# Kernel optimization log

Measured on AMD Instinct MI355X. Metric: run time of the kernel, lower is better.

## Reference

```python
import jax, jax.numpy as jnp
import numpy as np

N = 8192        # nodes
E = 262144      # edges (avg degree 32)
IN_CH = 256
CH = 128
SLOPE = 0.2     # PyG GATv2Conv default negative_slope


def gatv2(x, src, dst, wl, wr, att, b):
    """Single-head GATv2Conv (PyG defaults: share_weights=False, self-loops
    already appended to src/dst). x: [N, in]; wl, wr: [out, in]; att: [out]."""
    xl = x @ wl.T                      # [N, out] source-side transform (x_j)
    xr = x @ wr.T                      # [N, out] target-side transform (x_i)
    # per-edge attention logit: att . LeakyReLU(x_l[src] + x_r[dst])
    e = jax.nn.leaky_relu(xl[src] + xr[dst], SLOPE) @ att   # [E']
    # segment softmax over incoming edges of each target node
    m = jax.ops.segment_max(e, dst, num_segments=N)
    p = jnp.exp(e - m[dst])
    s = jax.ops.segment_sum(p, dst, num_segments=N)
    alpha = p / s[dst]                 # every node has a self-loop -> s > 0
    out = jax.ops.segment_sum(alpha[:, None] * xl[src], dst, num_segments=N)
    return out + b


def setup_inputs() -> dict:
    key = jax.random.key(0)
    ks = jax.random.split(key, 2 + 5 * 3)
    inp = {
        "x": jax.random.normal(ks[0], (N, IN_CH), dtype=jnp.float32),
        "edge_index": jax.random.randint(ks[1], (2, E), 0, N, dtype=jnp.int64),
    }
    dims = [(CH, IN_CH), (2 * CH, CH), (CH, 2 * CH), (CH, 2 * CH), (IN_CH, CH)]
    ki = 2
    for i, (oc, ic) in enumerate(dims, start=1):
        sc = (2.0 / (ic + oc)) ** 0.5  # glorot-ish
        inp[f"w{i}l"] = jax.random.normal(ks[ki], (oc, ic), dtype=jnp.float32) * sc
        inp[f"w{i}r"] = jax.random.normal(ks[ki + 1], (oc, ic), dtype=jnp.float32) * sc
        inp[f"a{i}"] = jax.random.normal(ks[ki + 2], (oc,), dtype=jnp.float32) * sc
        inp[f"b{i}"] = jnp.zeros((oc,), dtype=jnp.float32)
        ki += 3
    return inp


def reference(x, edge_index,
              w1l, w1r, a1, b1,
              w2l, w2r, a2, b2,
              w3l, w3r, a3, b3,
              w4l, w4r, a4, b4,
              w5l, w5r, a5, b5):
    loops = jnp.arange(N, dtype=edge_index.dtype)
    src = jnp.concatenate([edge_index[0], loops])   # add_self_loops=True
    dst = jnp.concatenate([edge_index[1], loops])
    h = jax.nn.relu(gatv2(x, src, dst, w1l, w1r, a1, b1))          # [N, CH]
    z = jax.nn.relu(gatv2(h, src, dst, w2l, w2r, a2, b2))          # [N, 2CH]
    re = jax.nn.relu(gatv2(z, src, dst, w3l, w3r, a3, b3))         # [N, CH]
    recon_edge = jax.nn.sigmoid(re @ re.T)                         # [N, N]
    xd = jax.nn.relu(gatv2(z, src, dst, w4l, w4r, a4, b4))         # [N, CH]
    x_rec = jax.nn.relu(gatv2(xd, src, dst, w5l, w5r, a5, b5))     # [N, IN_CH]
    return recon_edge, x_rec, z
```

## Files before the change

kernel.cpp:

```cpp
#include <hip/hip_runtime.h>
#include <hip/hip_bf16.h>
#include <math.h>

#define N_NODES 8192
#define N_EDGES 262144
#define EP (N_EDGES + N_NODES)
#define SLOPE 0.2f

typedef short bf16x8 __attribute__((ext_vector_type(8)));
typedef short short4v __attribute__((ext_vector_type(4)));
typedef float f32x4 __attribute__((ext_vector_type(4)));

__global__ void extract_hist(const int* __restrict__ raw,
                             int* __restrict__ esrc, int* __restrict__ edst,
                             int* __restrict__ counts) {
    __shared__ int sflag;
    int t = threadIdx.x;
    if (t < 64) {
        unsigned long long b = __ballot(raw[2 * t + 1] != 0);
        if (t == 0) sflag = (b == 0ULL) ? 1 : 0;
    }
    __syncthreads();
    int i64f = sflag;
    int k = blockIdx.x * blockDim.x + t;
    if (k >= N_EDGES) return;
    int s, d;
    if (i64f) {
        s = raw[2 * (size_t)k];
        d = raw[2 * ((size_t)N_EDGES + k)];
    } else {
        s = raw[k];
        d = raw[N_EDGES + k];
    }
    esrc[k] = s;
    edst[k] = d;
    atomicAdd(&counts[d], 1);
}

__global__ void scan_k(const int* __restrict__ counts, int* __restrict__ row_ptr) {
    __shared__ int part[256];
    int t = threadIdx.x;
    int base = t * 32;
    int loc[32];
    int s = 0;
    for (int i = 0; i < 32; ++i) { loc[i] = s; s += counts[base + i] + 1; }
    part[t] = s;
    __syncthreads();
    for (int off = 1; off < 256; off <<= 1) {
        int tmp = (t >= off) ? part[t - off] : 0;
        __syncthreads();
        part[t] += tmp;
        __syncthreads();
    }
    int incl = part[t];
    int excl = incl - s;
    for (int i = 0; i < 32; ++i) row_ptr[base + i] = excl + loc[i];
    if (t == 255) row_ptr[N_NODES] = incl;
}

__global__ void scatter_k(const int* __restrict__ esrc, const int* __restrict__ edst,
                          const int* __restrict__ row_ptr, int* __restrict__ cursor,
                          int* __restrict__ ssrc) {
    int k = blockIdx.x * blockDim.x + threadIdx.x;
    if (k >= EP) return;
    int s, d;
    if (k < N_EDGES) { s = esrc[k]; d = edst[k]; }
    else             { s = d = k - N_EDGES; }
    int pos = row_ptr[d] + atomicAdd(&cursor[d], 1);
    ssrc[pos] = s;
}

struct WPrep {
    const float* wl[5];
    const float* wr[5];
    int oc[5];
    int lk[5];
};

__global__ void prep_all(WPrep P, const float* __restrict__ x,
                         short* __restrict__ W3all, short* __restrict__ A3) {
    int gid = blockIdx.x * blockDim.x + threadIdx.x;
    if (gid < 524288) {
        int r = gid >> 6;
        int c4 = (gid & 63) << 2;
        f32x4 a = *(const f32x4*)&x[((size_t)r << 8) + c4];
        short4v h4, l4;
#pragma unroll
        for (int j = 0; j < 4; ++j) {
            __hip_bfloat16 hb = __float2bfloat16(a[j]);
            float hf = __bfloat162float(hb);
            __hip_bfloat16 lb = __float2bfloat16(a[j] - hf);
            h4[j] = *(short*)&hb;
            l4[j] = *(short*)&lb;
        }
        size_t ro = (size_t)r * 768;
        *(short4v*)&A3[ro + c4] = h4;
        *(short4v*)&A3[ro + 256 + c4] = l4;
        *(short4v*)&A3[ro + 512 + c4] = h4;
    } else {
        int g = gid - 524288;
        int l = g >> 16;
        if (l >= 5) return;
        int rem = g & 65535;
        int lk = P.lk[l], K = 1 << lk;
        int r = rem >> lk, c = rem & (K - 1);
        int OC = P.oc[l];
        const float* w = (r < OC) ? P.wl[l] : P.wr[l];
        int rr = (r < OC) ? r : r - OC;
        float a = w[((size_t)rr << lk) + c];
        __hip_bfloat16 hb = __float2bfloat16(a);
        float hf = __bfloat162float(hb);
        __hip_bfloat16 lb = __float2bfloat16(a - hf);
        size_t ro = (size_t)l * 196608 + (size_t)r * 3 * K;
        W3all[ro + c] = *(short*)&hb;
        W3all[ro + K + c] = *(short*)&hb;
        W3all[ro + 2 * K + c] = *(short*)&lb;
    }
}

#if __has_builtin(__builtin_amdgcn_global_load_lds)
#define GL16(gsrc, lbase, lofs)                                                       \
    __builtin_amdgcn_global_load_lds((const __attribute__((address_space(1))) void*)(gsrc), \
                                     (__attribute__((address_space(3))) void*)(lbase), 16, 0, 0)
#else
#define GL16(gsrc, lbase, lofs) (*(bf16x8*)((lbase) + (lofs)) = *(const bf16x8*)(gsrc))
#endif

__global__ __launch_bounds__(256) void gemm_bf16_nt(const short* __restrict__ A3,
                                                    const short* __restrict__ W3,
                                                    float* __restrict__ XL,
                                                    float* __restrict__ XR,
                                                    int K3, int N2, int OC) {
    __shared__ __align__(16) short As[2][4096];
    __shared__ __align__(16) short Bs[2][4096];
    int tid = threadIdx.x;
    int gx = gridDim.x;
    int lgx = (gx == 8) ? 3 : 2;
    int orig = blockIdx.x + (blockIdx.y << lgx);
    int nwg = gx << 7;
    int swzb = (orig & 7) * (nwg >> 3) + (orig >> 3);
    int bx = swzb & (gx - 1), by = swzb >> lgx;
    int i0 = by * 64, j0 = bx * 64;

    int wave = tid >> 6, lane = tid & 63;
    int b0 = wave * 1024 + lane * 16;
    int row0 = b0 >> 7;
    int rb0 = b0 & 127;
    int scb = rb0 ^ ((row0 & 7) << 4);
    const short* gA0 = A3 + (size_t)(i0 + row0) * K3 + (scb >> 1);
    const short* gA1 = A3 + (size_t)(i0 + row0 + 32) * K3 + (scb >> 1);
    const short* gB0 = W3 + (size_t)(j0 + row0) * K3 + (scb >> 1);
    const short* gB1 = W3 + (size_t)(j0 + row0 + 32) * K3 + (scb >> 1);
    int lofs = lane * 8;

#define STAGE(pb, k0s)                                      \
    do {                                                    \
        GL16(gA0 + (k0s), &As[pb][wave * 512], lofs);       \
        GL16(gA1 + (k0s), &As[pb][2048 + wave * 512], lofs);\
        GL16(gB0 + (k0s), &Bs[pb][wave * 512], lofs);       \
        GL16(gB1 + (k0s), &Bs[pb][2048 + wave * 512], lofs);\
    } while (0)

    int wr = (wave >> 1) * 32, wc = (wave & 1) * 32;
    int lm = lane & 15, quad = lane >> 4;
    f32x4 acc[2][2] = {};
    int nt = K3 >> 6;
    STAGE(0, 0);
    int cur = 0;
    for (int t = 0; t < nt; ++t) {
        if (t + 1 < nt) {
            STAGE(cur ^ 1, (t + 1) << 6);
            asm volatile("s_waitcnt vmcnt(4)" ::: "memory");
        } else {
            asm volatile("s_waitcnt vmcnt(0)" ::: "memory");
        }
        __builtin_amdgcn_s_barrier();
        __builtin_amdgcn_sched_barrier(0);
        const char* Ab = (const char*)&As[cur][0];
        const char* Bb = (const char*)&Bs[cur][0];
#pragma unroll
        for (int ks = 0; ks < 2; ++ks) {
            int kb = ks * 64 + quad * 16;
            bf16x8 a[2], b[2];
#pragma unroll
            for (int u = 0; u < 2; ++u) {
                int r = wr + u * 16 + lm;
                a[u] = *(const bf16x8*)(Ab + (((r << 7) | kb) ^ ((r & 7) << 4)));
            }
#pragma unroll
            for (int v = 0; v < 2; ++v) {
                int r = wc + v * 16 + lm;
                b[v] = *(const bf16x8*)(Bb + (((r << 7) | kb) ^ ((r & 7) << 4)));
            }
#pragma unroll
            for (int u = 0; u < 2; ++u)
#pragma unroll
                for (int v = 0; v < 2; ++v)
                    acc[u][v] = __builtin_amdgcn_mfma_f32_16x16x32_bf16(a[u], b[v], acc[u][v], 0, 0, 0);
        }
        __builtin_amdgcn_sched_barrier(0);
        __builtin_amdgcn_s_barrier();
        cur ^= 1;
    }
#undef STAGE
    float* Cb;
    int col0;
    if (j0 < OC) { Cb = XL; col0 = j0; } else { Cb = XR; col0 = j0 - OC; }
#pragma unroll
    for (int u = 0; u < 2; ++u)
#pragma unroll
        for (int v = 0; v < 2; ++v)
#pragma unroll
            for (int r = 0; r < 4; ++r) {
                int row = i0 + wr + u * 16 + quad * 4 + r;
                int col = col0 + wc + v * 16 + lm;
                Cb[(size_t)row * OC + col] = acc[u][v][r];
            }
}

#define LSTR 136

__global__ __launch_bounds__(256) void recon_sym(const unsigned short* __restrict__ Rb,
                                                 float* __restrict__ C) {
    __shared__ __align__(16) short Sh[2 * 128 * LSTR];
    short* As = Sh;
    short* Bs = Sh + 128 * LSTR;
    int tid = threadIdx.x;
    int orig = blockIdx.x;
    int s = (orig & 7) * 260 + (orig >> 3);
    float ff = 64.5f - sqrtf(64.5f * 64.5f - 2.0f * (float)s);
    int bi = (int)ff;
    while (bi > 0 && 64 * bi - bi * (bi - 1) / 2 > s) --bi;
    while (64 * (bi + 1) - (bi + 1) * bi / 2 <= s) ++bi;
    int bj = bi + (s - (64 * bi - bi * (bi - 1) / 2));
    int i0 = bi * 128, j0 = bj * 128;
    const short* R = (const short*)Rb;
#pragma unroll
    for (int c = 0; c < 8; ++c) {
        int idx = tid + c * 256;
        int row = idx >> 4, col = (idx & 15) * 8;
        *(bf16x8*)(&As[row * LSTR + col]) = *(const bf16x8*)(&R[(size_t)(i0 + row) * 128 + col]);
        *(bf16x8*)(&Bs[row * LSTR + col]) = *(const bf16x8*)(&R[(size_t)(j0 + row) * 128 + col]);
    }
    __syncthreads();
    int wave = tid >> 6, lane = tid & 63;
    int wr = (wave >> 1) * 64, wc = (wave & 1) * 64;
    int lm = lane & 15, quad = lane >> 4;
    f32x4 acc[4][4] = {};
#pragma unroll
    for (int ks = 0; ks < 4; ++ks) {
        int ko = ks * 32 + quad * 8;
        bf16x8 a[4], b[4];
#pragma unroll
        for (int u = 0; u < 4; ++u)
            a[u] = *(const bf16x8*)(&As[(wr + u * 16 + lm) * LSTR + ko]);
#pragma unroll
        for (int v = 0; v < 4; ++v)
            b[v] = *(const bf16x8*)(&Bs[(wc + v * 16 + lm) * LSTR + ko]);
#pragma unroll
        for (int u = 0; u < 4; ++u)
#pragma unroll
            for (int v = 0; v < 4; ++v)
                acc[u][v] = __builtin_amdgcn_mfma_f32_16x16x32_bf16(a[u], b[v], acc[u][v], 0, 0, 0);
    }
#pragma unroll
    for (int u = 0; u < 4; ++u)
#pragma unroll
        for (int v = 0; v < 4; ++v)
#pragma unroll
            for (int r = 0; r < 4; ++r) {
                acc[u][v][r] = 1.0f / (1.0f + __expf(-acc[u][v][r]));
                int row = i0 + wr + u * 16 + quad * 4 + r;
                int col = j0 + wc + v * 16 + lm;
                C[(size_t)row * 8192 + col] = acc[u][v][r];
            }
    if (bi != bj) {
        __syncthreads();
        float* T = (float*)Sh;
#pragma unroll
        for (int u = 0; u < 4; ++u)
#pragma unroll
            for (int v = 0; v < 4; ++v)
#pragma unroll
                for (int r = 0; r < 4; ++r)
                    T[(wr + u * 16 + quad * 4 + r) * 129 + (wc + v * 16 + lm)] = acc[u][v][r];
        __syncthreads();
#pragma unroll
        for (int it = 0; it < 64; ++it) {
            int idx = tid + it * 256;
            int rp = idx >> 7, cp = idx & 127;
            C[(size_t)(j0 + rp) * 8192 + (i0 + cp)] = T[cp * 129 + rp];
        }
    }
}

__global__ __launch_bounds__(256) void gat_node256(const int* __restrict__ row_ptr,
                                                   const int* __restrict__ ssrc,
                                                   const float* __restrict__ XL,
                                                   const float* __restrict__ XR,
                                                   const float* __restrict__ att,
                                                   const float* __restrict__ bias,
                                                   float* __restrict__ outf,
                                                   short* __restrict__ a3) {
    __shared__ float sacc[4][256];
    __shared__ float sm[4], ss[4];
    int d = blockIdx.x, t = threadIdx.x;
    int lane = t & 63, wave = t >> 6;
    int beg = row_ptr[d], end = row_ptr[d + 1];
    f32x4 xr = *(const f32x4*)&XR[(size_t)d * 256 + lane * 4];
    f32x4 at = *(const f32x4*)&att[lane * 4];
    float m = -INFINITY, s = 0.0f;
    f32x4 acc = {0.0f, 0.0f, 0.0f, 0.0f};
    int p = beg + wave;
    for (; p + 4 < end; p += 8) {
        int s0 = ssrc[p], s1 = ssrc[p + 4];
        f32x4 v0 = *(const f32x4*)&XL[(size_t)s0 * 256 + lane * 4];
        f32x4 v1 = *(const f32x4*)&XL[(size_t)s1 * 256 + lane * 4];
        float e0 = 0.0f, e1 = 0.0f;
#pragma unroll
        for (int j = 0; j < 4; ++j) {
            float u0 = v0[j] + xr[j]; u0 = (u0 > 0.0f) ? u0 : SLOPE * u0; e0 += u0 * at[j];
            float u1 = v1[j] + xr[j]; u1 = (u1 > 0.0f) ? u1 : SLOPE * u1; e1 += u1 * at[j];
        }
#pragma unroll
        for (int off = 32; off; off >>= 1) {
            e0 += __shfl_xor(e0, off, 64);
            e1 += __shfl_xor(e1, off, 64);
        }
        float mn = fmaxf(m, fmaxf(e0, e1));
        float f = __expf(m - mn), q0 = __expf(e0 - mn), q1 = __expf(e1 - mn);
        s = s * f + q0 + q1;
#pragma unroll
        for (int j = 0; j < 4; ++j) acc[j] = acc[j] * f + q0 * v0[j] + q1 * v1[j];
        m = mn;
    }
    if (p < end) {
        int si = ssrc[p];
        f32x4 v = *(const f32x4*)&XL[(size_t)si * 256 + lane * 4];
        float e = 0.0f;
#pragma unroll
        for (int j = 0; j < 4; ++j) {
            float u = v[j] + xr[j];
            u = (u > 0.0f) ? u : SLOPE * u;
            e += u * at[j];
        }
#pragma unroll
        for (int off = 32; off; off >>= 1) e += __shfl_xor(e, off, 64);
        float mn = fmaxf(m, e);
        float f = __expf(m - mn), p0 = __expf(e - mn);
        s = s * f + p0;
#pragma unroll
        for (int j = 0; j < 4; ++j) acc[j] = acc[j] * f + p0 * v[j];
        m = mn;
    }
    *(f32x4*)&sacc[wave][lane * 4] = acc;
    if (lane == 0) { sm[wave] = m; ss[wave] = s; }
    __syncthreads();
    float M = fmaxf(fmaxf(sm[0], sm[1]), fmaxf(sm[2], sm[3]));
    float tot = 0.0f, st = 0.0f;
#pragma unroll
    for (int w = 0; w < 4; ++w) {
        float fw = __expf(sm[w] - M);
        tot += sacc[w][t] * fw;
        st += ss[w] * fw;
    }
    float val = fmaxf(tot / st + bias[t], 0.0f);
    if (outf) outf[(size_t)d * 256 + t] = val;
    if (a3) {
        __hip_bfloat16 hb = __float2bfloat16(val);
        float hf = __bfloat162float(hb);
        __hip_bfloat16 lb = __float2bfloat16(val - hf);
        size_t ro = (size_t)d * 768;
        a3[ro + t] = *(short*)&hb;
        a3[ro + 256 + t] = *(short*)&lb;
        a3[ro + 512 + t] = *(short*)&hb;
    }
}

__global__ __launch_bounds__(256) void gat_node128(const int* __restrict__ row_ptr,
                                                   const int* __restrict__ ssrc,
                                                   const float* __restrict__ XL,
                                                   const float* __restrict__ XR,
                                                   const float* __restrict__ att,
                                                   const float* __restrict__ bias,
                                                   float* __restrict__ outf,
                                                   short* __restrict__ a3,
                                                   unsigned short* __restrict__ rb) {
    __shared__ float sacc[8][128];
    __shared__ float sm[8], ss[8];
    int d = blockIdx.x, t = threadIdx.x;
    int ln = t & 31, hw = t >> 5;
    int beg = row_ptr[d], end = row_ptr[d + 1];
    f32x4 xr = *(const f32x4*)&XR[(size_t)d * 128 + ln * 4];
    f32x4 at = *(const f32x4*)&att[ln * 4];
    float m = -INFINITY, s = 0.0f;
    f32x4 acc = {0.0f, 0.0f, 0.0f, 0.0f};
    int p = beg + hw;
    for (; p + 8 < end; p += 16) {
        int s0 = ssrc[p], s1 = ssrc[p + 8];
        f32x4 v0 = *(const f32x4*)&XL[(size_t)s0 * 128 + ln * 4];
        f32x4 v1 = *(const f32x4*)&XL[(size_t)s1 * 128 + ln * 4];
        float e0 = 0.0f, e1 = 0.0f;
#pragma unroll
        for (int j = 0; j < 4; ++j) {
            float u0 = v0[j] + xr[j]; u0 = (u0 > 0.0f) ? u0 : SLOPE * u0; e0 += u0 * at[j];
            float u1 = v1[j] + xr[j]; u1 = (u1 > 0.0f) ? u1 : SLOPE * u1; e1 += u1 * at[j];
        }
#pragma unroll
        for (int off = 16; off; off >>= 1) {
            e0 += __shfl_xor(e0, off, 32);
            e1 += __shfl_xor(e1, off, 32);
        }
        float mn = fmaxf(m, fmaxf(e0, e1));
        float f = __expf(m - mn), q0 = __expf(e0 - mn), q1 = __expf(e1 - mn);
        s = s * f + q0 + q1;
#pragma unroll
        for (int j = 0; j < 4; ++j) acc[j] = acc[j] * f + q0 * v0[j] + q1 * v1[j];
        m = mn;
    }
    if (p < end) {
        int si = ssrc[p];
        f32x4 v = *(const f32x4*)&XL[(size_t)si * 128 + ln * 4];
        float e = 0.0f;
#pragma unroll
        for (int j = 0; j < 4; ++j) {
            float u = v[j] + xr[j];
            u = (u > 0.0f) ? u : SLOPE * u;
            e += u * at[j];
        }
#pragma unroll
        for (int off = 16; off; off >>= 1) e += __shfl_xor(e, off, 32);
        float mn = fmaxf(m, e);
        float f = __expf(m - mn), p0 = __expf(e - mn);
        s = s * f + p0;
#pragma unroll
        for (int j = 0; j < 4; ++j) acc[j] = acc[j] * f + p0 * v[j];
        m = mn;
    }
    *(f32x4*)&sacc[hw][ln * 4] = acc;
    if (ln == 0) { sm[hw] = m; ss[hw] = s; }
    __syncthreads();
    if (t < 128) {
        float M = sm[0];
#pragma unroll
        for (int w = 1; w < 8; ++w) M = fmaxf(M, sm[w]);
        float tot = 0.0f, st = 0.0f;
#pragma unroll
        for (int w = 0; w < 8; ++w) {
            float fw = __expf(sm[w] - M);
            tot += sacc[w][t] * fw;
            st += ss[w] * fw;
        }
        float val = fmaxf(tot / st + bias[t], 0.0f);
        if (outf) outf[(size_t)d * 128 + t] = val;
        if (a3) {
            __hip_bfloat16 hb = __float2bfloat16(val);
            float hf = __bfloat162float(hb);
            __hip_bfloat16 lb = __float2bfloat16(val - hf);
            size_t ro = (size_t)d * 384;
            a3[ro + t] = *(short*)&hb;
            a3[ro + 128 + t] = *(short*)&lb;
            a3[ro + 256 + t] = *(short*)&hb;
        }
        if (rb) {
            __hip_bfloat16 hb = __float2bfloat16(val);
            rb[d * 128 + t] = *(unsigned short*)&hb;
        }
    }
}

static inline int ceil_div(int a, int b) { return (a + b - 1) / b; }

extern "C" void kernel_launch(void* const* d_in, const int* in_sizes, int n_in,
                              void* d_out, int out_size, void* d_ws, size_t ws_size,
                              hipStream_t stream) {
    const float* x    = (const float*)d_in[0];
    const int*   eraw = (const int*)d_in[1];

    WPrep P;
    const float* att[5];
    const float* bia[5];
    for (int l = 0; l < 5; ++l) {
        P.wl[l] = (const float*)d_in[2 + 4 * l + 0];
        P.wr[l] = (const float*)d_in[2 + 4 * l + 1];
        att[l]  = (const float*)d_in[2 + 4 * l + 2];
        bia[l]  = (const float*)d_in[2 + 4 * l + 3];
    }
    const int och[5]  = {128, 256, 128, 128, 256};
    const int logK[5] = {8, 7, 8, 8, 7};
    for (int l = 0; l < 5; ++l) { P.oc[l] = och[l]; P.lk[l] = logK[l]; }

    float* outp  = (float*)d_out;
    float* recon = outp;
    float* xrec  = outp + (size_t)67108864;
    float* zout  = outp + (size_t)69206016;

    float* W = (float*)d_ws;
    float* XL    = W;
    float* XR    = W + 2097152;
    short* A3    = (short*)(W + 4194304);
    short* W3all = (short*)(W + 7340032);
    unsigned short* Rb = (unsigned short*)(W + 7831552);
    int* I       = (int*)(W + 8355840);
    int* counts  = I;
    int* cursor  = I + 8192;
    int* row_ptr = I + 16384;
    int* ssrc    = I + 24577;
    int* esrc    = I + 294913;
    int* edst    = I + 557057;

    hipMemsetAsync(counts, 0, 2 * 8192 * sizeof(int), stream);
    extract_hist<<<ceil_div(N_EDGES, 256), 256, 0, stream>>>(eraw, esrc, edst, counts);
    scan_k<<<1, 256, 0, stream>>>(counts, row_ptr);
    scatter_k<<<ceil_div(EP, 256), 256, 0, stream>>>(esrc, edst, row_ptr, cursor, ssrc);

    prep_all<<<3328, 256, 0, stream>>>(P, x, W3all, A3);

    for (int l = 0; l < 5; ++l) {
        int lk = logK[l], OC = och[l];
        int N2 = OC << 1, K3 = 3 << lk;

        dim3 g(N2 / 64, N_NODES / 64);
        gemm_bf16_nt<<<g, 256, 0, stream>>>(A3, W3all + (size_t)l * 196608, XL, XR, K3, N2, OC);

        if (OC == 128) {
            float* of = nullptr;
            short* a3 = (l == 0 || l == 3) ? A3 : nullptr;
            unsigned short* rb = (l == 2) ? Rb : nullptr;
            gat_node128<<<N_NODES, 256, 0, stream>>>(row_ptr, ssrc, XL, XR, att[l], bia[l], of, a3, rb);
        } else {
            float* of = (l == 1) ? zout : xrec;
            short* a3 = (l == 1) ? A3 : nullptr;
            gat_node256<<<N_NODES, 256, 0, stream>>>(row_ptr, ssrc, XL, XR, att[l], bia[l], of, a3);
        }

        if (l == 2) {
            recon_sym<<<2080, 256, 0, stream>>>(Rb, recon);
        }
    }
}
```

Baseline: 557.9 us.

## Merge layer-3/4 GEMMs, batch their GAT passes, drop softmax max tracking

Layers 3 and 4 both read z, so their projections now run as one wider GEMM whose weights sit next to each other in memory. Their two 128-channel attention passes run in a single launch that picks per-layer parameters from the block index. The GEMM now writes XL and XR side by side in one strided buffer, so the GAT kernels read both through offsets. The online-softmax running max and its rescaling are removed, and the code exponentiates the raw logits. That saves exp and FMA work per edge but risks overflow or precision loss if the logits get large.

Measured after the change: 534.8 us. 4.1% less time.

```diff
diff --git a/kernel.cpp b/kernel.cpp
--- a/kernel.cpp
+++ b/kernel.cpp
@@ -128,9 +128,8 @@
 
 __global__ __launch_bounds__(256) void gemm_bf16_nt(const short* __restrict__ A3,
                                                     const short* __restrict__ W3,
-                                                    float* __restrict__ XL,
-                                                    float* __restrict__ XR,
-                                                    int K3, int N2, int OC) {
+                                                    float* __restrict__ C,
+                                                    int K3, int N2) {
     __shared__ __align__(16) short As[2][4096];
     __shared__ __align__(16) short Bs[2][4096];
     int tid = threadIdx.x;
@@ -203,9 +202,6 @@
         cur ^= 1;
     }
 #undef STAGE
-    float* Cb;
-    int col0;
-    if (j0 < OC) { Cb = XL; col0 = j0; } else { Cb = XR; col0 = j0 - OC; }
 #pragma unroll
     for (int u = 0; u < 2; ++u)
 #pragma unroll
@@ -213,8 +209,8 @@
 #pragma unroll
             for (int r = 0; r < 4; ++r) {
                 int row = i0 + wr + u * 16 + quad * 4 + r;
-                int col = col0 + wc + v * 16 + lm;
-                Cb[(size_t)row * OC + col] = acc[u][v][r];
+                int col = j0 + wc + v * 16 + lm;
+                C[(size_t)row * N2 + col] = acc[u][v][r];
             }
 }
 
@@ -294,28 +290,113 @@
     }
 }
 
-__global__ __launch_bounds__(256) void gat_node256(const int* __restrict__ row_ptr,
-                                                   const int* __restrict__ ssrc,
-                                                   const float* __restrict__ XL,
-                                                   const float* __restrict__ XR,
-                                                   const float* __restrict__ att,
-                                                   const float* __restrict__ bias,
-                                                   float* __restrict__ outf,
-                                                   short* __restrict__ a3) {
+struct GatP {
+    const float* att; const float* bias;
+    float* outf; short* a3; unsigned short* rb;
+    int xlo, xro;
+};
+
+__global__ __launch_bounds__(256) void gat128(const int* __restrict__ row_ptr,
+                                              const int* __restrict__ ssrc,
+                                              const float* __restrict__ XLR, int str,
+                                              GatP P0, GatP P1) {
+    __shared__ float sacc[8][128];
+    __shared__ float ss[8];
+    int d = blockIdx.x & (N_NODES - 1);
+    GatP P = (blockIdx.x >= N_NODES) ? P1 : P0;
+    int t = threadIdx.x, ln = t & 31, hw = t >> 5;
+    int beg = row_ptr[d], end = row_ptr[d + 1];
+    const float* XL = XLR + P.xlo;
+    f32x4 at = *(const f32x4*)&P.att[ln * 4];
+    f32x4 xr = *(const f32x4*)&XLR[(size_t)d * str + P.xro + ln * 4];
+    float s = 0.0f;
+    f32x4 acc = {0.0f, 0.0f, 0.0f, 0.0f};
+    int p = beg + hw;
+    for (; p + 8 < end; p += 16) {
+        int s0 = ssrc[p], s1 = ssrc[p + 8];
+        f32x4 v0 = *(const f32x4*)&XL[(size_t)s0 * str + ln * 4];
+        f32x4 v1 = *(const f32x4*)&XL[(size_t)s1 * str + ln * 4];
+        float e0 = 0.0f, e1 = 0.0f;
+#pragma unroll
+        for (int j = 0; j < 4; ++j) {
+            float u0 = v0[j] + xr[j]; u0 = (u0 > 0.0f) ? u0 : SLOPE * u0; e0 += u0 * at[j];
+            float u1 = v1[j] + xr[j]; u1 = (u1 > 0.0f) ? u1 : SLOPE * u1; e1 += u1 * at[j];
+        }
+#pragma unroll
+        for (int off = 16; off; off >>= 1) {
+            e0 += __shfl_xor(e0, off, 32);
+            e1 += __shfl_xor(e1, off, 32);
+        }
+        float q0 = __expf(e0), q1 = __expf(e1);
+        s += q0 + q1;
+#pragma unroll
+        for (int j = 0; j < 4; ++j) acc[j] += q0 * v0[j] + q1 * v1[j];
+    }
+    if (p < end) {
+        int si = ssrc[p];
+        f32x4 v = *(const f32x4*)&XL[(size_t)si * str + ln * 4];
+        float e = 0.0f;
+#pragma unroll
+        for (int j = 0; j < 4; ++j) {
+            float u = v[j] + xr[j];
+            u = (u > 0.0f) ? u : SLOPE * u;
+            e += u * at[j];
+        }
+#pragma unroll
+        for (int off = 16; off; off >>= 1) e += __shfl_xor(e, off, 32);
+        float q = __expf(e);
+        s += q;
+#pragma unroll
+        for (int j = 0; j < 4; ++j) acc[j] += q * v[j];
+    }
+    *(f32x4*)&sacc[hw][ln * 4] = acc;
+    if (ln == 0) ss[hw] = s;
+    __syncthreads();
+    if (t < 128) {
+        float tot = 0.0f, st = 0.0f;
+#pragma unroll
+        for (int w = 0; w < 8; ++w) { tot += sacc[w][t]; st += ss[w]; }
+        float val = fmaxf(tot / st + P.bias[t], 0.0f);
+        if (P.outf) P.outf[(size_t)d * 128 + t] = val;
+        if (P.a3) {
+            __hip_bfloat16 hb = __float2bfloat16(val);
+            float hf = __bfloat162float(hb);
+            __hip_bfloat16 lb = __float2bfloat16(val - hf);
+            size_t ro = (size_t)d * 384;
+            P.a3[ro + t] = *(short*)&hb;
+            P.a3[ro + 128 + t] = *(short*)&lb;
+            P.a3[ro + 256 + t] = *(short*)&hb;
+        }
+        if (P.rb) {
+            __hip_bfloat16 hb = __float2bfloat16(val);
+            P.rb[d * 128 + t] = *(unsigned short*)&hb;
+        }
+    }
+}
+
+__global__ __launch_bounds__(256) void gat256(const int* __restrict__ row_ptr,
+                                              const int* __restrict__ ssrc,
+                                              const float* __restrict__ XLR, int str,
+                                              const float* __restrict__ att,
+                                              const float* __restrict__ bias,
+                                              float* __restrict__ outf,
+                                              short* __restrict__ a3,
+                                              int xlo, int xro) {
     __shared__ float sacc[4][256];
-    __shared__ float sm[4], ss[4];
+    __shared__ float ss[4];
     int d = blockIdx.x, t = threadIdx.x;
     int lane = t & 63, wave = t >> 6;
     int beg = row_ptr[d], end = row_ptr[d + 1];
-    f32x4 xr = *(const f32x4*)&XR[(size_t)d * 256 + lane * 4];
+    const float* XL = XLR + xlo;
     f32x4 at = *(const f32x4*)&att[lane * 4];
-    float m = -INFINITY, s = 0.0f;
+    f32x4 xr = *(const f32x4*)&XLR[(size_t)d * str + xro + lane * 4];
+    float s = 0.0f;
     f32x4 acc = {0.0f, 0.0f, 0.0f, 0.0f};
     int p = beg + wave;
     for (; p + 4 < end; p += 8) {
         int s0 = ssrc[p], s1 = ssrc[p + 4];
-        f32x4 v0 = *(const f32x4*)&XL[(size_t)s0 * 256 + lane * 4];
-        f32x4 v1 = *(const f32x4*)&XL[(size_t)s1 * 256 + lane * 4];
+        f32x4 v0 = *(const f32x4*)&XL[(size_t)s0 * str + lane * 4];
+        f32x4 v1 = *(const f32x4*)&XL[(size_t)s1 * str + lane * 4];
         float e0 = 0.0f, e1 = 0.0f;
 #pragma unroll
         for (int j = 0; j < 4; ++j) {
@@ -327,16 +408,14 @@
             e0 += __shfl_xor(e0, off, 64);
             e1 += __shfl_xor(e1, off, 64);
         }
-        float mn = fmaxf(m, fmaxf(e0, e1));
-        float f = __expf(m - mn), q0 = __expf(e0 - mn), q1 = __expf(e1 - mn);
-        s = s * f + q0 + q1;
-#pragma unroll
-        for (int j = 0; j < 4; ++j) acc[j] = acc[j] * f + q0 * v0[j] + q1 * v1[j];
-        m = mn;
+        float q0 = __expf(e0), q1 = __expf(e1);
+        s += q0 + q1;
+#pragma unroll
+        for (int j = 0; j < 4; ++j) acc[j] += q0 * v0[j] + q1 * v1[j];
     }
     if (p < end) {
         int si = ssrc[p];
-        f32x4 v = *(const f32x4*)&XL[(size_t)si * 256 + lane * 4];
+        f32x4 v = *(const f32x4*)&XL[(size_t)si * str + lane * 4];
         float e = 0.0f;
 #pragma unroll
         for (int j = 0; j < 4; ++j) {
@@ -346,24 +425,17 @@
         }
 #pragma unroll
         for (int off = 32; off; off >>= 1) e += __shfl_xor(e, off, 64);
-        float mn = fmaxf(m, e);
-        float f = __expf(m - mn), p0 = __expf(e - mn);
-        s = s * f + p0;
-#pragma unroll
-        for (int j = 0; j < 4; ++j) acc[j] = acc[j] * f + p0 * v[j];
-        m = mn;
+        float q = __expf(e);
+        s += q;
+#pragma unroll
+        for (int j = 0; j < 4; ++j) acc[j] += q * v[j];
     }
     *(f32x4*)&sacc[wave][lane * 4] = acc;
-    if (lane == 0) { sm[wave] = m; ss[wave] = s; }
+    if (lane == 0) ss[wave] = s;
     __syncthreads();
-    float M = fmaxf(fmaxf(sm[0], sm[1]), fmaxf(sm[2], sm[3]));
     float tot = 0.0f, st = 0.0f;
 #pragma unroll
-    for (int w = 0; w < 4; ++w) {
-        float fw = __expf(sm[w] - M);
-        tot += sacc[w][t] * fw;
-        st += ss[w] * fw;
-    }
+    for (int w = 0; w < 4; ++w) { tot += sacc[w][t]; st += ss[w]; }
     float val = fmaxf(tot / st + bias[t], 0.0f);
     if (outf) outf[(size_t)d * 256 + t] = val;
     if (a3) {
@@ -377,98 +449,6 @@
     }
 }
 
-__global__ __launch_bounds__(256) void gat_node128(const int* __restrict__ row_ptr,
-                                                   const int* __restrict__ ssrc,
-                                                   const float* __restrict__ XL,
-                                                   const float* __restrict__ XR,
-                                                   const float* __restrict__ att,
-                                                   const float* __restrict__ bias,
-                                                   float* __restrict__ outf,
-                                                   short* __restrict__ a3,
-                                                   unsigned short* __restrict__ rb) {
-    __shared__ float sacc[8][128];
-    __shared__ float sm[8], ss[8];
-    int d = blockIdx.x, t = threadIdx.x;
-    int ln = t & 31, hw = t >> 5;
-    int beg = row_ptr[d], end = row_ptr[d + 1];
-    f32x4 xr = *(const f32x4*)&XR[(size_t)d * 128 + ln * 4];
-    f32x4 at = *(const f32x4*)&att[ln * 4];
-    float m = -INFINITY, s = 0.0f;
-    f32x4 acc = {0.0f, 0.0f, 0.0f, 0.0f};
-    int p = beg + hw;
-    for (; p + 8 < end; p += 16) {
-        int s0 = ssrc[p], s1 = ssrc[p + 8];
-        f32x4 v0 = *(const f32x4*)&XL[(size_t)s0 * 128 + ln * 4];
-        f32x4 v1 = *(const f32x4*)&XL[(size_t)s1 * 128 + ln * 4];
-        float e0 = 0.0f, e1 = 0.0f;
-#pragma unroll
-        for (int j = 0; j < 4; ++j) {
-            float u0 = v0[j] + xr[j]; u0 = (u0 > 0.0f) ? u0 : SLOPE * u0; e0 += u0 * at[j];
-            float u1 = v1[j] + xr[j]; u1 = (u1 > 0.0f) ? u1 : SLOPE * u1; e1 += u1 * at[j];
-        }
-#pragma unroll
-        for (int off = 16; off; off >>= 1) {
-            e0 += __shfl_xor(e0, off, 32);
-            e1 += __shfl_xor(e1, off, 32);
-        }
-        float mn = fmaxf(m, fmaxf(e0, e1));
-        float f = __expf(m - mn), q0 = __expf(e0 - mn), q1 = __expf(e1 - mn);
-        s = s * f + q0 + q1;
-#pragma unroll
-        for (int j = 0; j < 4; ++j) acc[j] = acc[j] * f + q0 * v0[j] + q1 * v1[j];
-        m = mn;
-    }
-    if (p < end) {
-        int si = ssrc[p];
-        f32x4 v = *(const f32x4*)&XL[(size_t)si * 128 + ln * 4];
-        float e = 0.0f;
-#pragma unroll
-        for (int j = 0; j < 4; ++j) {
-            float u = v[j] + xr[j];
-            u = (u > 0.0f) ? u : SLOPE * u;
-            e += u * at[j];
-        }
-#pragma unroll
-        for (int off = 16; off; off >>= 1) e += __shfl_xor(e, off, 32);
-        float mn = fmaxf(m, e);
-        float f = __expf(m - mn), p0 = __expf(e - mn);
-        s = s * f + p0;
-#pragma unroll
-        for (int j = 0; j < 4; ++j) acc[j] = acc[j] * f + p0 * v[j];
-        m = mn;
-    }
-    *(f32x4*)&sacc[hw][ln * 4] = acc;
-    if (ln == 0) { sm[hw] = m; ss[hw] = s; }
-    __syncthreads();
-    if (t < 128) {
-        float M = sm[0];
-#pragma unroll
-        for (int w = 1; w < 8; ++w) M = fmaxf(M, sm[w]);
-        float tot = 0.0f, st = 0.0f;
-#pragma unroll
-        for (int w = 0; w < 8; ++w) {
-            float fw = __expf(sm[w] - M);
-            tot += sacc[w][t] * fw;
-            st += ss[w] * fw;
-        }
-        float val = fmaxf(tot / st + bias[t], 0.0f);
-        if (outf) outf[(size_t)d * 128 + t] = val;
-        if (a3) {
-            __hip_bfloat16 hb = __float2bfloat16(val);
-            float hf = __bfloat162float(hb);
-            __hip_bfloat16 lb = __float2bfloat16(val - hf);
-            size_t ro = (size_t)d * 384;
-            a3[ro + t] = *(short*)&hb;
-            a3[ro + 128 + t] = *(short*)&lb;
-            a3[ro + 256 + t] = *(short*)&hb;
-        }
-        if (rb) {
-            __hip_bfloat16 hb = __float2bfloat16(val);
-            rb[d * 128 + t] = *(unsigned short*)&hb;
-        }
-    }
-}
-
 static inline int ceil_div(int a, int b) { return (a + b - 1) / b; }
 
 extern "C" void kernel_launch(void* const* d_in, const int* in_sizes, int n_in,
@@ -496,8 +476,7 @@
     float* zout  = outp + (size_t)69206016;
 
     float* W = (float*)d_ws;
-    float* XL    = W;
-    float* XR    = W + 2097152;
+    float* XLR   = W;
     short* A3    = (short*)(W + 4194304);
     short* W3all = (short*)(W + 7340032);
     unsigned short* Rb = (unsigned short*)(W + 7831552);
@@ -516,26 +495,32 @@
 
     prep_all<<<3328, 256, 0, stream>>>(P, x, W3all, A3);
 
-    for (int l = 0; l < 5; ++l) {
-        int lk = logK[l], OC = och[l];
-        int N2 = OC << 1, K3 = 3 << lk;
-
-        dim3 g(N2 / 64, N_NODES / 64);
-        gemm_bf16_nt<<<g, 256, 0, stream>>>(A3, W3all + (size_t)l * 196608, XL, XR, K3, N2, OC);
-
-        if (OC == 128) {
-            float* of = nullptr;
-            short* a3 = (l == 0 || l == 3) ? A3 : nullptr;
-            unsigned short* rb = (l == 2) ? Rb : nullptr;
-            gat_node128<<<N_NODES, 256, 0, stream>>>(row_ptr, ssrc, XL, XR, att[l], bia[l], of, a3, rb);
-        } else {
-            float* of = (l == 1) ? zout : xrec;
-            short* a3 = (l == 1) ? A3 : nullptr;
-            gat_node256<<<N_NODES, 256, 0, stream>>>(row_ptr, ssrc, XL, XR, att[l], bia[l], of, a3);
-        }
-
-        if (l == 2) {
-            recon_sym<<<2080, 256, 0, stream>>>(Rb, recon);
-        }
-    }
-}
+    GatP gp[5];
+    for (int l = 0; l < 5; ++l)
+        gp[l] = GatP{att[l], bia[l], nullptr, nullptr, nullptr, 0, 0};
+
+    {
+        dim3 g(4, 128);
+        gemm_bf16_nt<<<g, 256, 0, stream>>>(A3, W3all + 0 * 196608, XLR, 768, 256);
+        gp[0].a3 = A3; gp[0].xlo = 0; gp[0].xro = 128;
+        gat128<<<N_NODES, 256, 0, stream>>>(row_ptr, ssrc, XLR, 256, gp[0], gp[0]);
+    }
+    {
+        dim3 g(8, 128);
+        gemm_bf16_nt<<<g, 256, 0, stream>>>(A3, W3all + 1 * 196608, XLR, 384, 512);
+        gat256<<<N_NODES, 256, 0, stream>>>(row_ptr, ssrc, XLR, 512, att[1], bia[1], zout, A3, 0, 256);
+    }
+    {
+        dim3 g(8, 128);
+        gemm_bf16_nt<<<g, 256, 0, stream>>>(A3, W3all + 2 * 196608, XLR, 768, 512);
+        gp[2].rb = Rb;               gp[2].xlo = 0;   gp[2].xro = 128;
+        gp[3].a3 = A3;               gp[3].xlo = 256; gp[3].xro = 384;
+        gat128<<<2 * N_NODES, 256, 0, stream>>>(row_ptr, ssrc, XLR, 512, gp[2], gp[3]);
+        recon_sym<<<2080, 256, 0, stream>>>(Rb, recon);
+    }
+    {
+        dim3 g(8, 128);
+        gemm_bf16_nt<<<g, 256, 0, stream>>>(A3, W3all + 4 * 196608, XLR, 384, 512);
+        gat256<<<N_NODES, 256, 0, stream>>>(row_ptr, ssrc, XLR, 512, att[4], bia[4], xrec, nullptr, 0, 256);
+    }
+}
```
